# Kernel tuning notes

Measured on AMD Instinct MI355X. Metric: run time of the kernel, lower is better.

Reference implementation:

```python
import jax, jax.numpy as jnp
import numpy as np

GROUP_SIZE = 32
FP8_MAX = 448.0
EPS = 1e-8


def fp8_pseudo_quantize_groupwise(x):
    """Per-group (contiguous groups of GROUP_SIZE along last dim) fp8-e4m3
    pseudo-quantization: scale to fp8 range, cast to fp8, cast back, rescale."""
    shape = x.shape
    g = shape[-1] // GROUP_SIZE
    xg = x.reshape(*shape[:-1], g, GROUP_SIZE)
    amax = jnp.max(jnp.abs(xg), axis=-1, keepdims=True)
    scale = jnp.maximum(amax, EPS) / FP8_MAX  # fp32 per-group scale
    q = (xg / scale).astype(jnp.float8_e4m3fn).astype(x.dtype)
    return (q * scale).reshape(shape)


def setup_inputs() -> dict:
    key = jax.random.key(0)
    k1, k2, k3 = jax.random.split(key, 3)
    B, S, K, N = 4, 2048, 4096, 4096
    x = jax.random.normal(k1, (B, S, K), dtype=jnp.float32)
    # Linear-like init scale for weight/bias
    W = jax.random.normal(k2, (N, K), dtype=jnp.float32) * (1.0 / np.sqrt(K))
    bias = jax.random.normal(k3, (N,), dtype=jnp.float32) * (1.0 / np.sqrt(K))
    return {"x": x, "W": W, "bias": bias}


def reference(x, W, bias):
    # pseudo mode, a_bit=8 < 16: quantize both activations and weight
    Wq = fp8_pseudo_quantize_groupwise(W)   # [N, K]
    xq = fp8_pseudo_quantize_groupwise(x)   # [B, S, K]
    # F.linear: xq @ Wq.T + bias
    out = jnp.einsum('bsk,nk->bsn', xq, Wq) + bias
    return out
```

## Files before the change

### kernel.cpp

```cpp
#include <hip/hip_runtime.h>
#include <hip/hip_bf16.h>

typedef __bf16 bf16x8 __attribute__((ext_vector_type(8)));
typedef float floatx4 __attribute__((ext_vector_type(4)));
typedef unsigned short ushortx8 __attribute__((ext_vector_type(8)));

#define FP8_MAX 448.0f
#define QEPS 1e-8f

#define GLLDS16(gptr, lptr)                                                          \
  __builtin_amdgcn_global_load_lds((const __attribute__((address_space(1))) void*)(gptr), \
                                   (__attribute__((address_space(3))) void*)(lptr), 16, 0, 0)

__global__ __launch_bounds__(256) void quant_dq_kernel(
    const float* __restrict__ src, __hip_bfloat16* __restrict__ dst, long long n)
{
    long long t = (long long)blockIdx.x * blockDim.x + threadIdx.x;
    long long base = t * 8;
    if (base >= n) return;

    const float4 v0 = *(const float4*)(src + base);
    const float4 v1 = *(const float4*)(src + base + 4);

    float am = fmaxf(
        fmaxf(fmaxf(fabsf(v0.x), fabsf(v0.y)), fmaxf(fabsf(v0.z), fabsf(v0.w))),
        fmaxf(fmaxf(fabsf(v1.x), fabsf(v1.y)), fmaxf(fabsf(v1.z), fabsf(v1.w))));
    am = fmaxf(am, __shfl_xor(am, 1));
    am = fmaxf(am, __shfl_xor(am, 2));
    const float scale = fmaxf(am, QEPS) / FP8_MAX;

    int p0 = __builtin_amdgcn_cvt_pk_fp8_f32(v0.x / scale, v0.y / scale, 0, false);
    int p1 = __builtin_amdgcn_cvt_pk_fp8_f32(v0.z / scale, v0.w / scale, 0, false);
    int p2 = __builtin_amdgcn_cvt_pk_fp8_f32(v1.x / scale, v1.y / scale, 0, false);
    int p3 = __builtin_amdgcn_cvt_pk_fp8_f32(v1.z / scale, v1.w / scale, 0, false);

    float r0 = __builtin_amdgcn_cvt_f32_fp8(p0, 0) * scale;
    float r1 = __builtin_amdgcn_cvt_f32_fp8(p0, 1) * scale;
    float r2 = __builtin_amdgcn_cvt_f32_fp8(p1, 0) * scale;
    float r3 = __builtin_amdgcn_cvt_f32_fp8(p1, 1) * scale;
    float r4 = __builtin_amdgcn_cvt_f32_fp8(p2, 0) * scale;
    float r5 = __builtin_amdgcn_cvt_f32_fp8(p2, 1) * scale;
    float r6 = __builtin_amdgcn_cvt_f32_fp8(p3, 0) * scale;
    float r7 = __builtin_amdgcn_cvt_f32_fp8(p3, 1) * scale;

    alignas(16) __hip_bfloat16 hb[8] = {
        __float2bfloat16(r0), __float2bfloat16(r1),
        __float2bfloat16(r2), __float2bfloat16(r3),
        __float2bfloat16(r4), __float2bfloat16(r5),
        __float2bfloat16(r6), __float2bfloat16(r7)};
    *(ushortx8*)(dst + base) = *(const ushortx8*)hb;
}

__global__ __launch_bounds__(256, 2) void gemm_bias_kernel(
    const __hip_bfloat16* __restrict__ A,
    const __hip_bfloat16* __restrict__ B,
    const float* __restrict__ bias,
    float* __restrict__ C,
    int M, int N, int K)
{
    __shared__ __attribute__((aligned(16))) __hip_bfloat16 As[128 * 32];
    __shared__ __attribute__((aligned(16))) __hip_bfloat16 Bs[128 * 32];

    const int tid  = threadIdx.x;
    const int lane = tid & 63;
    const int wave = tid >> 6;
    const int wr   = (wave >> 1) * 64;
    const int wc   = (wave & 1) * 64;

    const long bm = (long)blockIdx.y * 128;
    const long bn = (long)blockIdx.x * 128;

    const int srow = tid >> 2;
    const int scol = (tid & 3) * 8;

    const __hip_bfloat16* gA0 = A + (bm + srow) * (long)K + scol;
    const __hip_bfloat16* gA1 = A + (bm + 64 + srow) * (long)K + scol;
    const __hip_bfloat16* gB0 = B + (bn + srow) * (long)K + scol;
    const __hip_bfloat16* gB1 = B + (bn + 64 + srow) * (long)K + scol;

    __hip_bfloat16* lA0 = As + tid * 8;
    __hip_bfloat16* lA1 = As + 2048 + tid * 8;
    __hip_bfloat16* lB0 = Bs + tid * 8;
    __hip_bfloat16* lB1 = Bs + 2048 + tid * 8;

    floatx4 acc[4][4];
#pragma unroll
    for (int i = 0; i < 4; ++i)
#pragma unroll
        for (int j = 0; j < 4; ++j)
            acc[i][j] = (floatx4){0.f, 0.f, 0.f, 0.f};

    const int fr = lane & 15;
    const int fk = (lane >> 4) * 8;

    for (int k0 = 0; k0 < K; k0 += 32) {
        GLLDS16(gA0 + k0, lA0);
        GLLDS16(gA1 + k0, lA1);
        GLLDS16(gB0 + k0, lB0);
        GLLDS16(gB1 + k0, lB1);
        __syncthreads();

        bf16x8 af[4], bfv[4];
#pragma unroll
        for (int i = 0; i < 4; ++i)
            af[i] = *(const bf16x8*)(As + (wr + i * 16 + fr) * 32 + fk);
#pragma unroll
        for (int j = 0; j < 4; ++j)
            bfv[j] = *(const bf16x8*)(Bs + (wc + j * 16 + fr) * 32 + fk);

#pragma unroll
        for (int i = 0; i < 4; ++i)
#pragma unroll
            for (int j = 0; j < 4; ++j)
                acc[i][j] = __builtin_amdgcn_mfma_f32_16x16x32_bf16(af[i], bfv[j], acc[i][j], 0, 0, 0);
        __syncthreads();
    }

    const int rq = (lane >> 4) * 4;
#pragma unroll
    for (int j = 0; j < 4; ++j) {
        const long gc = bn + wc + j * 16 + fr;
        const float bj = bias[gc];
#pragma unroll
        for (int i = 0; i < 4; ++i) {
            const long gr = bm + wr + i * 16 + rq;
            float* cp = C + gr * (long)N + gc;
#pragma unroll
            for (int r = 0; r < 4; ++r)
                cp[(long)r * N] = acc[i][j][r] + bj;
        }
    }
}

extern "C" void kernel_launch(void* const* d_in, const int* in_sizes, int n_in,
                              void* d_out, int out_size, void* d_ws, size_t ws_size,
                              hipStream_t stream) {
    const float* x    = (const float*)d_in[0];
    const float* W    = (const float*)d_in[1];
    const float* bias = (const float*)d_in[2];
    float* out = (float*)d_out;

    const long long nx = in_sizes[0];
    const long long nw = in_sizes[1];
    const int N = in_sizes[2];
    const int K = (int)(nw / N);
    const int M = (int)(nx / K);

    __hip_bfloat16* xq = (__hip_bfloat16*)d_ws;
    __hip_bfloat16* wq = xq + nx;

    {
        long long tx = nx / 8;
        int blocks = (int)((tx + 255) / 256);
        quant_dq_kernel<<<blocks, 256, 0, stream>>>(x, xq, nx);
    }
    {
        long long tw = nw / 8;
        int blocks = (int)((tw + 255) / 256);
        quant_dq_kernel<<<blocks, 256, 0, stream>>>(W, wq, nw);
    }

    dim3 grid(N / 128, M / 128);
    gemm_bias_kernel<<<grid, 256, 0, stream>>>(xq, wq, bias, out, M, N, K);
}
```

Baseline: 556.7 us.

## Double GEMM K-tile to 64 with XOR-swizzled LDS layout

Raises the per-iteration K tile from 32 to 64, which halves the number of barrier pairs and global-to-LDS load rounds per output tile. The LDS layout gets an XOR swizzle on the 16-byte column group, applied on the global source address so the direct global_load_lds writes stay linear, and matched on the fragment reads to avoid bank conflicts. LDS use doubles to 32 KB per block, which may reduce occupancy, and there is still no double buffering.

```diff
diff --git a/kernel.cpp b/kernel.cpp
--- a/kernel.cpp
+++ b/kernel.cpp
@@ -58,8 +58,8 @@
     float* __restrict__ C,
     int M, int N, int K)
 {
-    __shared__ __attribute__((aligned(16))) __hip_bfloat16 As[128 * 32];
-    __shared__ __attribute__((aligned(16))) __hip_bfloat16 Bs[128 * 32];
+    __shared__ __attribute__((aligned(16))) __hip_bfloat16 As[128 * 64];
+    __shared__ __attribute__((aligned(16))) __hip_bfloat16 Bs[128 * 64];
 
     const int tid  = threadIdx.x;
     const int lane = tid & 63;
@@ -70,18 +70,15 @@
     const long bm = (long)blockIdx.y * 128;
     const long bn = (long)blockIdx.x * 128;
 
-    const int srow = tid >> 2;
-    const int scol = (tid & 3) * 8;
+    const int srow = tid >> 3;
+    const int scg  = (tid & 7) ^ (srow & 7);
 
-    const __hip_bfloat16* gA0 = A + (bm + srow) * (long)K + scol;
-    const __hip_bfloat16* gA1 = A + (bm + 64 + srow) * (long)K + scol;
-    const __hip_bfloat16* gB0 = B + (bn + srow) * (long)K + scol;
-    const __hip_bfloat16* gB1 = B + (bn + 64 + srow) * (long)K + scol;
+    const __hip_bfloat16* gA = A + (bm + srow) * (long)K + scg * 8;
+    const __hip_bfloat16* gB = B + (bn + srow) * (long)K + scg * 8;
+    const long rstep = 32 * (long)K;
 
-    __hip_bfloat16* lA0 = As + tid * 8;
-    __hip_bfloat16* lA1 = As + 2048 + tid * 8;
-    __hip_bfloat16* lB0 = Bs + tid * 8;
-    __hip_bfloat16* lB1 = Bs + 2048 + tid * 8;
+    __hip_bfloat16* lA = As + tid * 8;
+    __hip_bfloat16* lB = Bs + tid * 8;
 
     floatx4 acc[4][4];
 #pragma unroll
@@ -91,28 +88,35 @@
             acc[i][j] = (floatx4){0.f, 0.f, 0.f, 0.f};
 
     const int fr = lane & 15;
-    const int fk = (lane >> 4) * 8;
+    const int fq = lane >> 4;
 
-    for (int k0 = 0; k0 < K; k0 += 32) {
-        GLLDS16(gA0 + k0, lA0);
-        GLLDS16(gA1 + k0, lA1);
-        GLLDS16(gB0 + k0, lB0);
-        GLLDS16(gB1 + k0, lB1);
+    for (int k0 = 0; k0 < K; k0 += 64) {
+#pragma unroll
+        for (int r = 0; r < 4; ++r) {
+            GLLDS16(gA + k0 + r * rstep, lA + r * 32 * 64);
+            GLLDS16(gB + k0 + r * rstep, lB + r * 32 * 64);
+        }
         __syncthreads();
 
-        bf16x8 af[4], bfv[4];
 #pragma unroll
-        for (int i = 0; i < 4; ++i)
-            af[i] = *(const bf16x8*)(As + (wr + i * 16 + fr) * 32 + fk);
+        for (int ks = 0; ks < 2; ++ks) {
+            bf16x8 af[4], bfv[4];
 #pragma unroll
-        for (int j = 0; j < 4; ++j)
-            bfv[j] = *(const bf16x8*)(Bs + (wc + j * 16 + fr) * 32 + fk);
-
+            for (int i = 0; i < 4; ++i) {
+                const int ra = wr + i * 16 + fr;
+                af[i] = *(const bf16x8*)(As + ra * 64 + (((ks * 4 + fq) ^ (ra & 7)) * 8));
+            }
 #pragma unroll
-        for (int i = 0; i < 4; ++i)
+            for (int j = 0; j < 4; ++j) {
+                const int rb = wc + j * 16 + fr;
+                bfv[j] = *(const bf16x8*)(Bs + rb * 64 + (((ks * 4 + fq) ^ (rb & 7)) * 8));
+            }
 #pragma unroll
-            for (int j = 0; j < 4; ++j)
-                acc[i][j] = __builtin_amdgcn_mfma_f32_16x16x32_bf16(af[i], bfv[j], acc[i][j], 0, 0, 0);
+            for (int i = 0; i < 4; ++i)
+#pragma unroll
+                for (int j = 0; j < 4; ++j)
+                    acc[i][j] = __builtin_amdgcn_mfma_f32_16x16x32_bf16(af[i], bfv[j], acc[i][j], 0, 0, 0);
+        }
         __syncthreads();
     }
 
```

Result: faster. 506.3 us (-9.1%).
